# Kernel optimization log

Hardware: AMD Instinct MI355X
Metric: run time of the kernel (lower is better)

The kernel has to match this reference:

```python
import jax, jax.numpy as jnp
import numpy as np

N = 50000   # num_nodes
H = 128     # n_hidden
C = 16      # num_classes
R = 8       # num_rels
B = 4       # num_bases
E = 800000  # num_edges


def setup_inputs() -> dict:
    key = jax.random.key(0)
    ks = jax.random.split(key, 20)
    s = 0.05
    return {
        "src": jax.random.randint(ks[0], (E,), 0, N),
        "dst": jax.random.randint(ks[1], (E,), 0, N),
        "h": jnp.arange(N),                      # node IDs (first layer in_feat == num_nodes)
        "r": jax.random.randint(ks[2], (E,), 0, R),
        "norm": jax.random.uniform(ks[3], (E, 1), dtype=jnp.float32),
        # layer 0: basis weights over [num_nodes -> H]
        "bases0": jax.random.normal(ks[4], (B, N, H), dtype=jnp.float32) * s,
        "wcomp0": jax.random.normal(ks[5], (R, B), dtype=jnp.float32) * s,
        "loop0": jax.random.normal(ks[6], (N, H), dtype=jnp.float32) * s,
        "bias0": jnp.zeros((H,), dtype=jnp.float32),
        # layer 1: H -> H
        "bases1": jax.random.normal(ks[7], (B, H, H), dtype=jnp.float32) * s,
        "wcomp1": jax.random.normal(ks[8], (R, B), dtype=jnp.float32) * s,
        "loop1": jax.random.normal(ks[9], (H, H), dtype=jnp.float32) * s,
        "bias1": jnp.zeros((H,), dtype=jnp.float32),
        # layer 2: H -> C
        "bases2": jax.random.normal(ks[10], (B, H, C), dtype=jnp.float32) * s,
        "wcomp2": jax.random.normal(ks[11], (R, B), dtype=jnp.float32) * s,
        "loop2": jax.random.normal(ks[12], (H, C), dtype=jnp.float32) * s,
        "bias2": jnp.zeros((C,), dtype=jnp.float32),
    }


def _agg(msg, dst):
    return jax.ops.segment_sum(msg, dst, num_segments=N)


def _layer_id(ids, src, dst, r, norm, bases, wcomp, loop, bias):
    # first layer: input features are node IDs -> embedding lookup into composed weight
    w = jnp.einsum('rb,bnf->rnf', wcomp, bases)      # [R, N, H]
    msg = w[r, ids[src]] * norm                      # [E, H] gather per edge
    out = _agg(msg, dst) + loop[ids] + bias          # aggregate + self-loop + bias
    return jax.nn.relu(out)


def _layer_dense(x, src, dst, r, norm, bases, wcomp, loop, bias, act):
    w = jnp.einsum('rb,bdf->rdf', wcomp, bases)      # [R, d_in, d_out]
    trans = jnp.einsum('nd,rdf->rnf', x, w)          # [R, N, d_out] (all rel transforms)
    msg = trans[r, src] * norm                       # [E, d_out] relation-indexed gather
    out = _agg(msg, dst) + x @ loop + bias
    return jax.nn.relu(out) if act else out


def reference(src, dst, h, r, norm,
              bases0, wcomp0, loop0, bias0,
              bases1, wcomp1, loop1, bias1,
              bases2, wcomp2, loop2, bias2):
    x = _layer_id(h, src, dst, r, norm, bases0, wcomp0, loop0, bias0)
    x = _layer_dense(x, src, dst, r, norm, bases1, wcomp1, loop1, bias1, act=True)
    x = _layer_dense(x, src, dst, r, norm, bases2, wcomp2, loop2, bias2, act=False)
    return x
```

## Files before the change

### kernel.cpp

```cpp
#include <hip/hip_runtime.h>

#define NN 50000
#define NP 50048
#define HH 128
#define CC 16
#define RRL 8
#define BB 4
#define EE 800000
#define NT (RRL * NN)
#define SCAN_CHUNK 2048
#define NBLK_SCAN ((NT + SCAN_CHUNK - 1) / SCAN_CHUNK)
#define KBIG 1152
#define W0B_BLOCKS ((NN * 32) / 256)
#define COMPOSE_THREADS (HH * KBIG + RRL * CC * HH + CC * HH)
#define COMPOSE_BLOCKS ((COMPOSE_THREADS + 255) / 256)
#define NC 98
#define SPLIT 2
#define CHUNK_E 4096
#define PA_BLOCKS ((EE + CHUNK_E - 1) / CHUNK_E)

typedef short bf16x8_t __attribute__((ext_vector_type(8)));
typedef float f32x4_t __attribute__((ext_vector_type(4)));

__device__ __forceinline__ unsigned short f2bf(float f) {
  unsigned int x = __float_as_uint(f);
  unsigned int r = x + 0x7fffu + ((x >> 16) & 1u);
  return (unsigned short)(r >> 16);
}
__device__ __forceinline__ float bflo(unsigned int u) { return __uint_as_float(u << 16); }
__device__ __forceinline__ float bfhi(unsigned int u) {
  return __uint_as_float(u & 0xffff0000u);
}
__device__ __forceinline__ void acc8(float* a, uint4 v, float nrm) {
  a[0] = fmaf(nrm, bflo(v.x), a[0]);
  a[1] = fmaf(nrm, bfhi(v.x), a[1]);
  a[2] = fmaf(nrm, bflo(v.y), a[2]);
  a[3] = fmaf(nrm, bfhi(v.y), a[3]);
  a[4] = fmaf(nrm, bflo(v.z), a[4]);
  a[5] = fmaf(nrm, bfhi(v.z), a[5]);
  a[6] = fmaf(nrm, bflo(v.w), a[6]);
  a[7] = fmaf(nrm, bfhi(v.w), a[7]);
}


__global__ __launch_bounds__(256) void hist2_kernel(const int* __restrict__ r,
                                                    const int* __restrict__ dst,
                                                    int* __restrict__ cnt) {
  int e = blockIdx.x * 256 + threadIdx.x;
  if (e < EE) atomicAdd(&cnt[dst[e] * RRL + r[e]], 1);
}

__global__ __launch_bounds__(256) void scanA_kernel(const int* __restrict__ cnt,
                                                    int* __restrict__ off,
                                                    int* __restrict__ partials) {
  __shared__ int sums[256];
  int tid = threadIdx.x;
  int base = blockIdx.x * SCAN_CHUNK + tid * 8;
  int v[8];
  int s = 0;
#pragma unroll
  for (int j = 0; j < 8; ++j) {
    int idx = base + j;
    v[j] = (idx < NT) ? cnt[idx] : 0;
    s += v[j];
  }
  sums[tid] = s;
  __syncthreads();
  for (int o = 1; o < 256; o <<= 1) {
    int t = (tid >= o) ? sums[tid - o] : 0;
    __syncthreads();
    sums[tid] += t;
    __syncthreads();
  }
  int run = sums[tid] - s;
#pragma unroll
  for (int j = 0; j < 8; ++j) {
    int idx = base + j;
    if (idx < NT) off[idx] = run;
    run += v[j];
  }
  if (tid == 255) partials[blockIdx.x] = sums[255];
}

__global__ __launch_bounds__(256) void scanB_kernel(const int* __restrict__ partials,
                                                    int* __restrict__ pexcl) {
  __shared__ int sums[256];
  int tid = threadIdx.x;
  int p = (tid < NBLK_SCAN) ? partials[tid] : 0;
  sums[tid] = p;
  __syncthreads();
  for (int o = 1; o < 256; o <<= 1) {
    int t = (tid >= o) ? sums[tid - o] : 0;
    __syncthreads();
    sums[tid] += t;
    __syncthreads();
  }
  if (tid < NBLK_SCAN) pexcl[tid] = sums[tid] - p;
}

__global__ __launch_bounds__(256) void addC_kernel(int* __restrict__ off,
                                                   const int* __restrict__ pexcl,
                                                   int* __restrict__ cur,
                                                   int* __restrict__ curC) {
  int tid = threadIdx.x;
  int add = pexcl[blockIdx.x];
  int base = blockIdx.x * SCAN_CHUNK + tid * 8;
#pragma unroll
  for (int j = 0; j < 8; ++j) {
    int idx = base + j;
    if (idx < NT) {
      int v = off[idx] + add;
      off[idx] = v;
      cur[idx] = v;
      if ((idx & 4095) == 0) curC[idx >> 12] = v;
    }
  }
  if (blockIdx.x == 0 && tid == 0) off[NT] = EE;
}


__global__ __launch_bounds__(256) void partitionA_kernel(
    const int* __restrict__ r, const int* __restrict__ dst, const int* __restrict__ src,
    const float* __restrict__ norm, int* __restrict__ curC, unsigned* __restrict__ tmpK,
    uint2* __restrict__ tmpP) {
  __shared__ int hist[NC];
  __shared__ int run[NC];
  int tid = threadIdx.x;
  int base = blockIdx.x * CHUNK_E;
  for (int i = tid; i < NC; i += 256) hist[i] = 0;
  __syncthreads();
#pragma unroll
  for (int j = 0; j < CHUNK_E / 256; ++j) {
    int e = base + tid + j * 256;
    if (e < EE) atomicAdd(&hist[dst[e] >> 9], 1);
  }
  __syncthreads();
  if (tid < NC && hist[tid] > 0) run[tid] = atomicAdd(&curC[tid], hist[tid]);
  __syncthreads();
#pragma unroll
  for (int j = 0; j < CHUNK_E / 256; ++j) {
    int e = base + tid + j * 256;
    if (e < EE) {
      int d = dst[e], z = r[e];
      int c = d >> 9;
      int pos = atomicAdd(&run[c], 1);
      tmpK[pos] = (unsigned)(d * RRL + z);
      uint2 pay;
      pay.x = (unsigned)src[e] | ((unsigned)z << 24);
      pay.y = __float_as_uint(norm[e]);
      tmpP[pos] = pay;
    }
  }
}


__global__ __launch_bounds__(256) void placeB_kernel(const int* __restrict__ off2,
                                                     const unsigned* __restrict__ tmpK,
                                                     const uint2* __restrict__ tmpP,
                                                     int* __restrict__ cur2,
                                                     uint2* __restrict__ ep1) {
  int c = blockIdx.x / SPLIT, q = blockIdx.x % SPLIT;
  int kb = c * 4096;
  int ke = (c + 1) * 4096;
  if (ke > NT) ke = NT;
  int beg = off2[kb], end = off2[ke];
  int len = end - beg;
  int qb = beg + (len * q) / SPLIT;
  int qe = beg + (len * (q + 1)) / SPLIT;
  for (int i = qb + threadIdx.x; i < qe; i += 256) {
    unsigned key = tmpK[i];
    uint2 pay = tmpP[i];
    int pos = atomicAdd(&cur2[key], 1);
    ep1[pos] = pay;
  }
}


__global__ __launch_bounds__(256) void prep_weights_kernel(
    const float* __restrict__ bases0, const float* __restrict__ wcomp0,
    unsigned short* __restrict__ w0b, const float* __restrict__ wcomp1,
    const float* __restrict__ bases1, const float* __restrict__ loop1,
    const float* __restrict__ wcomp2, const float* __restrict__ bases2,
    const float* __restrict__ loop2, unsigned short* __restrict__ w1big,
    unsigned short* __restrict__ w2t, unsigned short* __restrict__ loop2t) {
  if (blockIdx.x < W0B_BLOCKS) {
    int idx = blockIdx.x * 256 + threadIdx.x;
    int m = idx >> 5, c = idx & 31;
    if (m >= NN) return;
    float4 b0 = ((const float4*)(bases0 + ((size_t)0 * NN + m) * HH))[c];
    float4 b1 = ((const float4*)(bases0 + ((size_t)1 * NN + m) * HH))[c];
    float4 b2 = ((const float4*)(bases0 + ((size_t)2 * NN + m) * HH))[c];
    float4 b3 = ((const float4*)(bases0 + ((size_t)3 * NN + m) * HH))[c];
#pragma unroll
    for (int z = 0; z < RRL; ++z) {
      float c0 = wcomp0[z * BB + 0], c1 = wcomp0[z * BB + 1];
      float c2 = wcomp0[z * BB + 2], c3 = wcomp0[z * BB + 3];
      float vx = c0 * b0.x + c1 * b1.x + c2 * b2.x + c3 * b3.x;
      float vy = c0 * b0.y + c1 * b1.y + c2 * b2.y + c3 * b3.y;
      float vz = c0 * b0.z + c1 * b1.z + c2 * b2.z + c3 * b3.z;
      float vw = c0 * b0.w + c1 * b1.w + c2 * b2.w + c3 * b3.w;
      uint2 pk;
      pk.x = ((unsigned)f2bf(vy) << 16) | f2bf(vx);
      pk.y = ((unsigned)f2bf(vw) << 16) | f2bf(vz);
      ((uint2*)(w0b + ((size_t)z * NP + m) * HH))[c] = pk;
    }
    return;
  }
  int idx = (blockIdx.x - W0B_BLOCKS) * 256 + threadIdx.x;
  if (idx < HH * KBIG) {
    int n = idx / KBIG, k = idx - n * KBIG;
    float a;
    if (k < 1024) {
      int z = k >> 7, kk = k & 127;
      a = 0.f;
#pragma unroll
      for (int b = 0; b < BB; ++b)
        a += wcomp1[z * BB + b] * bases1[((size_t)b * HH + kk) * HH + n];
    } else {
      int kk = k - 1024;
      a = loop1[kk * HH + n];
    }
    w1big[idx] = f2bf(a);
    return;
  }
  int j = idx - HH * KBIG;
  if (j < RRL * CC * HH) {
    int z = j >> 11;
    int rem = j & 2047;
    int n = rem >> 7, k = rem & 127;
    float a = 0.f;
#pragma unroll
    for (int b = 0; b < BB; ++b)
      a += wcomp2[z * BB + b] * bases2[((size_t)b * HH + k) * CC + n];
    w2t[j] = f2bf(a);
    return;
  }
  j -= RRL * CC * HH;
  if (j < CC * HH) {
    int n = j >> 7, k = j & 127;
    loop2t[j] = f2bf(loop2[k * CC + n]);
  }
}


__global__ __launch_bounds__(256) void l0_seg_kernel(
    const int* __restrict__ h, const int* __restrict__ off2, const uint2* __restrict__ ep1,
    const unsigned short* __restrict__ w0b, const float* __restrict__ loop0,
    const float* __restrict__ bias0, unsigned short* __restrict__ x1b) {
  int lane = threadIdx.x & 63;
  int n = blockIdx.x * 4 + (threadIdx.x >> 6);
  if (n >= NP) return;
  const int g = lane >> 4;
  const int t = lane & 15;
  float acc[8];
#pragma unroll
  for (int j = 0; j < 8; ++j) acc[j] = 0.f;

  if (n < NN) {
    int beg = off2[n * RRL];
    int end = off2[n * RRL + RRL];
    int i = beg + g;
    uint2 p0 = {0u, 0u}, p1 = {0u, 0u};
    if (i < end) p0 = ep1[i];
    if (i + 4 < end) p1 = ep1[i + 4];
    unsigned r0 = (p0.x >> 24) * NP + (unsigned)h[p0.x & 0xFFFFFFu];
    unsigned r1 = (p1.x >> 24) * NP + (unsigned)h[p1.x & 0xFFFFFFu];
    while (i < end) {
      uint2 q0 = {0u, 0u}, q1 = {0u, 0u};
      if (i + 8 < end) q0 = ep1[i + 8];
      if (i + 12 < end) q1 = ep1[i + 12];
      uint4 va = *(const uint4*)(w0b + (size_t)r0 * HH + t * 8);
      uint4 vb = *(const uint4*)(w0b + (size_t)r1 * HH + t * 8);
      float na = __uint_as_float(p0.y), nb = __uint_as_float(p1.y);
      acc8(acc, va, na);
      acc8(acc, vb, nb);
      i += 8;
      p0 = q0;
      p1 = q1;
      r0 = (q0.x >> 24) * NP + (unsigned)h[q0.x & 0xFFFFFFu];
      r1 = (q1.x >> 24) * NP + (unsigned)h[q1.x & 0xFFFFFFu];
    }
  }
#pragma unroll
  for (int j = 0; j < 8; ++j) {
    acc[j] += __shfl_xor(acc[j], 16, 64);
    acc[j] += __shfl_xor(acc[j], 32, 64);
  }
  if (g != 0) return;
  uint4 o = {0u, 0u, 0u, 0u};
  if (n < NN) {
    int hn = h[n];
    float4 l0v = ((const float4*)(loop0 + (size_t)hn * HH))[t * 2];
    float4 l1v = ((const float4*)(loop0 + (size_t)hn * HH))[t * 2 + 1];
    float4 b0v = ((const float4*)bias0)[t * 2];
    float4 b1v = ((const float4*)bias0)[t * 2 + 1];
    float e0 = fmaxf(acc[0] + l0v.x + b0v.x, 0.f);
    float e1 = fmaxf(acc[1] + l0v.y + b0v.y, 0.f);
    float e2 = fmaxf(acc[2] + l0v.z + b0v.z, 0.f);
    float e3 = fmaxf(acc[3] + l0v.w + b0v.w, 0.f);
    float e4 = fmaxf(acc[4] + l1v.x + b1v.x, 0.f);
    float e5 = fmaxf(acc[5] + l1v.y + b1v.y, 0.f);
    float e6 = fmaxf(acc[6] + l1v.z + b1v.z, 0.f);
    float e7 = fmaxf(acc[7] + l1v.w + b1v.w, 0.f);
    o.x = ((unsigned)f2bf(e1) << 16) | f2bf(e0);
    o.y = ((unsigned)f2bf(e3) << 16) | f2bf(e2);
    o.z = ((unsigned)f2bf(e5) << 16) | f2bf(e4);
    o.w = ((unsigned)f2bf(e7) << 16) | f2bf(e6);
  }
  *(uint4*)(x1b + (size_t)n * HH + t * 8) = o;
}


__global__ __launch_bounds__(256) void l1_agg_kernel(const int* __restrict__ off2,
                                                     const uint2* __restrict__ ep1,
                                                     const unsigned short* __restrict__ x1b,
                                                     unsigned short* __restrict__ AGG) {
  int tid = threadIdx.x;
  int gid = blockIdx.x * 16 + (tid >> 4);
  int l = tid & 15;
  int n = gid >> 3, z = gid & 7;
  if (n >= NP) return;
  unsigned short* orow = AGG + (size_t)n * 1024 + z * 128 + l * 8;
  if (n >= NN) {
    *(uint4*)orow = (uint4){0u, 0u, 0u, 0u};
    return;
  }
  int beg = off2[gid];
  int end = off2[gid + 1];
  float a[8];
#pragma unroll
  for (int j = 0; j < 8; ++j) a[j] = 0.f;

  int i = beg;
  uint2 p0 = {0u, 0u}, p1 = {0u, 0u};
  if (i < end) p0 = ep1[i];
  if (i + 1 < end) p1 = ep1[i + 1];
  while (i < end) {
    uint2 q0 = {0u, 0u}, q1 = {0u, 0u};
    if (i + 2 < end) q0 = ep1[i + 2];
    if (i + 3 < end) q1 = ep1[i + 3];
    unsigned s0 = p0.x & 0xFFFFFFu, s1 = p1.x & 0xFFFFFFu;
    uint4 v0 = *(const uint4*)(x1b + (size_t)s0 * HH + l * 8);
    uint4 v1 = *(const uint4*)(x1b + (size_t)s1 * HH + l * 8);
    float n0 = __uint_as_float(p0.y), n1 = __uint_as_float(p1.y);
    acc8(a, v0, n0);
    acc8(a, v1, n1);
    i += 2;
    p0 = q0;
    p1 = q1;
  }
  uint4 o;
  o.x = ((unsigned)f2bf(a[1]) << 16) | f2bf(a[0]);
  o.y = ((unsigned)f2bf(a[3]) << 16) | f2bf(a[2]);
  o.z = ((unsigned)f2bf(a[5]) << 16) | f2bf(a[4]);
  o.w = ((unsigned)f2bf(a[7]) << 16) | f2bf(a[6]);
  *(uint4*)orow = o;
}


__global__ __launch_bounds__(256) void gemm_k1152_kernel(
    const unsigned short* __restrict__ AGG, const unsigned short* __restrict__ x1b,
    const unsigned short* __restrict__ w1big, const float* __restrict__ bias1,
    unsigned short* __restrict__ x2b) {
  constexpr int LP = 136;
  __shared__ unsigned short Alds[64 * LP];
  __shared__ unsigned short Blds[128 * LP];
  const int row0 = blockIdx.x * 64;
  const int tid = threadIdx.x;
  const int w = tid >> 6, lane = tid & 63;
  const int quad = lane >> 4, l15 = lane & 15;
  const int rb = (w >> 1) * 32;
  const int cb = (w & 1) * 64;

  f32x4_t acc[2][4];
#pragma unroll
  for (int rt = 0; rt < 2; ++rt)
#pragma unroll
    for (int ct = 0; ct < 4; ++ct) acc[rt][ct] = (f32x4_t){0.f, 0.f, 0.f, 0.f};

  for (int kb = 0; kb < 9; ++kb) {
    if (kb) __syncthreads();
#pragma unroll
    for (int it = 0; it < 4; ++it) {
      int flat = tid + it * 256;
      int row = flat >> 4, c8 = flat & 15;
      const unsigned short* srcp =
          (kb < 8) ? AGG + (size_t)(row0 + row) * 1024 + kb * 128 + c8 * 8
                   : x1b + (size_t)(row0 + row) * 128 + c8 * 8;
      *(uint4*)(&Alds[row * LP + c8 * 8]) = *(const uint4*)srcp;
    }
#pragma unroll
    for (int it = 0; it < 8; ++it) {
      int flat = tid + it * 256;
      int row = flat >> 4, c8 = flat & 15;
      *(uint4*)(&Blds[row * LP + c8 * 8]) =
          *(const uint4*)(w1big + (size_t)row * KBIG + kb * 128 + c8 * 8);
    }
    __syncthreads();
#pragma unroll
    for (int ks = 0; ks < 4; ++ks) {
      int ko = ks * 32 + quad * 8;
      bf16x8_t af[2], bfr[4];
#pragma unroll
      for (int rt = 0; rt < 2; ++rt)
        af[rt] = *(const bf16x8_t*)(&Alds[(rb + rt * 16 + l15) * LP + ko]);
#pragma unroll
      for (int ct = 0; ct < 4; ++ct)
        bfr[ct] = *(const bf16x8_t*)(&Blds[(cb + ct * 16 + l15) * LP + ko]);
#pragma unroll
      for (int rt = 0; rt < 2; ++rt)
#pragma unroll
        for (int ct = 0; ct < 4; ++ct)
          acc[rt][ct] =
              __builtin_amdgcn_mfma_f32_16x16x32_bf16(af[rt], bfr[ct], acc[rt][ct], 0, 0, 0);
    }
  }
#pragma unroll
  for (int rt = 0; rt < 2; ++rt)
#pragma unroll
    for (int ct = 0; ct < 4; ++ct) {
      int n = cb + ct * 16 + l15;
      float bv = bias1[n];
#pragma unroll
      for (int i = 0; i < 4; ++i) {
        int m = row0 + rb + rt * 16 + quad * 4 + i;
        float val = (m < NN) ? fmaxf(acc[rt][ct][i] + bv, 0.f) : 0.f;
        x2b[(size_t)m * HH + n] = f2bf(val);
      }
    }
}


__global__ __launch_bounds__(256) void l2_trans_kernel(
    const unsigned short* __restrict__ x2b, const unsigned short* __restrict__ w2t,
    const unsigned short* __restrict__ loop2t, const float* __restrict__ bias2,
    unsigned short* __restrict__ trans2, float* __restrict__ out) {
  constexpr int LP = 136;
  __shared__ unsigned short Alds[128 * LP];
  __shared__ unsigned short Blds[9][16 * LP];
  const int row0 = blockIdx.x * 128;
  const int tid = threadIdx.x;

#pragma unroll
  for (int it = 0; it < 8; ++it) {
    int flat = tid + it * 256;
    int row = flat >> 4, c8 = flat & 15;
    *(uint4*)(&Alds[row * LP + c8 * 8]) =
        *(const uint4*)(x2b + ((size_t)(row0 + row)) * 128 + c8 * 8);
  }
  {
    int row = tid >> 4, c8 = tid & 15;
#pragma unroll
    for (int z = 0; z < 9; ++z) {
      const unsigned short* B = (z < 8) ? w2t + (size_t)z * CC * HH : loop2t;
      *(uint4*)(&Blds[z][row * LP + c8 * 8]) = *(const uint4*)(B + row * 128 + c8 * 8);
    }
  }
  __syncthreads();

  const int w = tid >> 6, lane = tid & 63;
  const int quad = lane >> 4, l15 = lane & 15;
  const int rb = w * 32;

  for (int z = 0; z < 9; ++z) {
    f32x4_t acc[2];
    acc[0] = (f32x4_t){0.f, 0.f, 0.f, 0.f};
    acc[1] = (f32x4_t){0.f, 0.f, 0.f, 0.f};
#pragma unroll
    for (int ks = 0; ks < 4; ++ks) {
      int ko = ks * 32 + quad * 8;
      bf16x8_t af0 = *(const bf16x8_t*)(&Alds[(rb + l15) * LP + ko]);
      bf16x8_t af1 = *(const bf16x8_t*)(&Alds[(rb + 16 + l15) * LP + ko]);
      bf16x8_t bfr = *(const bf16x8_t*)(&Blds[z][l15 * LP + ko]);
      acc[0] = __builtin_amdgcn_mfma_f32_16x16x32_bf16(af0, bfr, acc[0], 0, 0, 0);
      acc[1] = __builtin_amdgcn_mfma_f32_16x16x32_bf16(af1, bfr, acc[1], 0, 0, 0);
    }
    if (z < 8) {
      unsigned short* ob = trans2 + (size_t)z * NP * CC;
#pragma unroll
      for (int rt = 0; rt < 2; ++rt)
#pragma unroll
        for (int i = 0; i < 4; ++i) {
          int m = row0 + rb + rt * 16 + quad * 4 + i;
          ob[(size_t)m * CC + l15] = f2bf(acc[rt][i]);
        }
    } else {
      float bv = bias2[l15];
#pragma unroll
      for (int rt = 0; rt < 2; ++rt)
#pragma unroll
        for (int i = 0; i < 4; ++i) {
          int m = row0 + rb + rt * 16 + quad * 4 + i;
          if (m < NN) out[(size_t)m * CC + l15] = acc[rt][i] + bv;
        }
    }
  }
}


__global__ __launch_bounds__(256) void l2_seg_kernel(const int* __restrict__ off2,
                                                     const uint2* __restrict__ ep1,
                                                     const unsigned short* __restrict__ trans2,
                                                     float* __restrict__ outp) {
  int lane = threadIdx.x & 63;
  int n = blockIdx.x * 4 + (threadIdx.x >> 6);
  if (n >= NN) return;
  const int g = lane >> 3;
  const int t = lane & 7;
  float a0 = 0.f, a1 = 0.f;
  int beg = off2[n * RRL];
  int end = off2[n * RRL + RRL];
  int i = beg + g;
  uint2 p0 = {0u, 0u}, p1 = {0u, 0u};
  if (i < end) p0 = ep1[i];
  if (i + 8 < end) p1 = ep1[i + 8];
  while (i < end) {
    uint2 q0 = {0u, 0u}, q1 = {0u, 0u};
    if (i + 16 < end) q0 = ep1[i + 16];
    if (i + 24 < end) q1 = ep1[i + 24];
    unsigned s0 = p0.x & 0xFFFFFFu, z0 = p0.x >> 24;
    unsigned s1 = p1.x & 0xFFFFFFu, z1 = p1.x >> 24;
    unsigned int u0 =
        *(const unsigned int*)(trans2 + ((size_t)z0 * NP + s0) * CC + t * 2);
    unsigned int u1 =
        *(const unsigned int*)(trans2 + ((size_t)z1 * NP + s1) * CC + t * 2);
    float na = __uint_as_float(p0.y), nb = __uint_as_float(p1.y);
    a0 = fmaf(na, bflo(u0), a0);
    a1 = fmaf(na, bfhi(u0), a1);
    a0 = fmaf(nb, bflo(u1), a0);
    a1 = fmaf(nb, bfhi(u1), a1);
    i += 16;
    p0 = q0;
    p1 = q1;
  }
  a0 += __shfl_xor(a0, 8, 64);
  a0 += __shfl_xor(a0, 16, 64);
  a0 += __shfl_xor(a0, 32, 64);
  a1 += __shfl_xor(a1, 8, 64);
  a1 += __shfl_xor(a1, 16, 64);
  a1 += __shfl_xor(a1, 32, 64);
  if (g != 0) return;
  float2* o = (float2*)(outp + (size_t)n * CC) + t;
  float2 cv = *o;
  cv.x += a0;
  cv.y += a1;
  *o = cv;
}


extern "C" void kernel_launch(void* const* d_in, const int* in_sizes, int n_in,
                              void* d_out, int out_size, void* d_ws, size_t ws_size,
                              hipStream_t stream) {
  const int* src = (const int*)d_in[0];
  const int* dst = (const int*)d_in[1];
  const int* h = (const int*)d_in[2];
  const int* r = (const int*)d_in[3];
  const float* norm = (const float*)d_in[4];
  const float* bases0 = (const float*)d_in[5];
  const float* wcomp0 = (const float*)d_in[6];
  const float* loop0 = (const float*)d_in[7];
  const float* bias0 = (const float*)d_in[8];
  const float* bases1 = (const float*)d_in[9];
  const float* wcomp1 = (const float*)d_in[10];
  const float* loop1 = (const float*)d_in[11];
  const float* bias1 = (const float*)d_in[12];
  const float* bases2 = (const float*)d_in[13];
  const float* wcomp2 = (const float*)d_in[14];
  const float* loop2 = (const float*)d_in[15];
  const float* bias2 = (const float*)d_in[16];
  float* out = (float*)d_out;

  char* p = (char*)d_ws;
  auto alloc = [&](size_t bytes) {
    char* q = p;
    p += (bytes + 255) & ~(size_t)255;
    return q;
  };
  unsigned short* x1b = (unsigned short*)alloc((size_t)NP * HH * 2);
  unsigned short* x2b = (unsigned short*)alloc((size_t)NP * HH * 2);
  unsigned short* trans2 = (unsigned short*)alloc((size_t)RRL * NP * CC * 2);
  unsigned short* w1big = (unsigned short*)alloc((size_t)HH * KBIG * 2);
  unsigned short* w2t = (unsigned short*)alloc((size_t)RRL * CC * HH * 2);
  unsigned short* loop2t = (unsigned short*)alloc((size_t)CC * HH * 2);
  uint2* ep1 = (uint2*)alloc((size_t)EE * 8);
  unsigned* tmpK = (unsigned*)alloc((size_t)EE * 4);
  uint2* tmpP = (uint2*)alloc((size_t)EE * 8);
  int* off2 = (int*)alloc((size_t)(NT + 1) * 4);
  int* cur2 = (int*)alloc((size_t)NT * 4);
  int* cnt2 = (int*)alloc((size_t)NT * 4);
  int* curC = (int*)alloc(1024);
  int* partials = (int*)alloc(1024);
  int* pexcl = (int*)alloc(1024);
  unsigned short* BIG = (unsigned short*)alloc((size_t)RRL * NP * HH * 2);

  hipMemsetAsync(cnt2, 0, (size_t)NT * 4, stream);
  hist2_kernel<<<(EE + 255) / 256, 256, 0, stream>>>(r, dst, cnt2);
  scanA_kernel<<<NBLK_SCAN, 256, 0, stream>>>(cnt2, off2, partials);
  scanB_kernel<<<1, 256, 0, stream>>>(partials, pexcl);
  addC_kernel<<<NBLK_SCAN, 256, 0, stream>>>(off2, pexcl, cur2, curC);
  partitionA_kernel<<<PA_BLOCKS, 256, 0, stream>>>(r, dst, src, norm, curC, tmpK, tmpP);
  placeB_kernel<<<NC * SPLIT, 256, 0, stream>>>(off2, tmpK, tmpP, cur2, ep1);

  prep_weights_kernel<<<W0B_BLOCKS + COMPOSE_BLOCKS, 256, 0, stream>>>(
      bases0, wcomp0, BIG, wcomp1, bases1, loop1, wcomp2, bases2, loop2, w1big, w2t,
      loop2t);

  l0_seg_kernel<<<NP / 4, 256, 0, stream>>>(h, off2, ep1, BIG, loop0, bias0, x1b);

  l1_agg_kernel<<<NP * 8 / 16, 256, 0, stream>>>(off2, ep1, x1b, BIG);
  gemm_k1152_kernel<<<NP / 64, 256, 0, stream>>>(BIG, x1b, w1big, bias1, x2b);

  l2_trans_kernel<<<NP / 128, 256, 0, stream>>>(x2b, w2t, loop2t, bias2, trans2, out);
  l2_seg_kernel<<<(NN + 3) / 4, 256, 0, stream>>>(off2, ep1, trans2, out);
}
```

Before: 479.0 us.

## Interleave layer-0 composed weights by node and widen per-lane gathers

Changes the composed layer-0 weight table from relation-major [R][NP][H] to node-major [N][R][H], so all eight relation rows of a source node sit contiguously. The prep kernel now has each thread handle 8 columns and emit one 16-byte store per relation. The gather kernel now has each lane load 32 bytes per edge and handle 8 edges per wave instead of 4, with an extra shuffle stage for the reduction. The aim is better locality and fewer, wider memory transactions for the random edge gathers, at the cost of higher register use and fewer edges in flight per lane group.

```diff
diff --git a/kernel.cpp b/kernel.cpp
--- a/kernel.cpp
+++ b/kernel.cpp
@@ -11,7 +11,7 @@
 #define SCAN_CHUNK 2048
 #define NBLK_SCAN ((NT + SCAN_CHUNK - 1) / SCAN_CHUNK)
 #define KBIG 1152
-#define W0B_BLOCKS ((NN * 32) / 256)
+#define W0B_BLOCKS ((NN * 16) / 256)
 #define COMPOSE_THREADS (HH * KBIG + RRL * CC * HH + CC * HH)
 #define COMPOSE_BLOCKS ((COMPOSE_THREADS + 255) / 256)
 #define NC 98
@@ -152,7 +152,6 @@
     }
   }
 }
-
 
 __global__ __launch_bounds__(256) void placeB_kernel(const int* __restrict__ off2,
                                                      const unsigned* __restrict__ tmpK,
@@ -185,24 +184,33 @@
     unsigned short* __restrict__ w2t, unsigned short* __restrict__ loop2t) {
   if (blockIdx.x < W0B_BLOCKS) {
     int idx = blockIdx.x * 256 + threadIdx.x;
-    int m = idx >> 5, c = idx & 31;
-    if (m >= NN) return;
-    float4 b0 = ((const float4*)(bases0 + ((size_t)0 * NN + m) * HH))[c];
-    float4 b1 = ((const float4*)(bases0 + ((size_t)1 * NN + m) * HH))[c];
-    float4 b2 = ((const float4*)(bases0 + ((size_t)2 * NN + m) * HH))[c];
-    float4 b3 = ((const float4*)(bases0 + ((size_t)3 * NN + m) * HH))[c];
+    int m = idx >> 4, c8 = idx & 15;
+    float4 a[BB][2];
+#pragma unroll
+    for (int b = 0; b < BB; ++b) {
+      const float4* sp = (const float4*)(bases0 + ((size_t)b * NN + m) * HH + c8 * 8);
+      a[b][0] = sp[0];
+      a[b][1] = sp[1];
+    }
+    uint4* orow = (uint4*)w0b + (size_t)m * 128 + c8;
 #pragma unroll
     for (int z = 0; z < RRL; ++z) {
       float c0 = wcomp0[z * BB + 0], c1 = wcomp0[z * BB + 1];
       float c2 = wcomp0[z * BB + 2], c3 = wcomp0[z * BB + 3];
-      float vx = c0 * b0.x + c1 * b1.x + c2 * b2.x + c3 * b3.x;
-      float vy = c0 * b0.y + c1 * b1.y + c2 * b2.y + c3 * b3.y;
-      float vz = c0 * b0.z + c1 * b1.z + c2 * b2.z + c3 * b3.z;
-      float vw = c0 * b0.w + c1 * b1.w + c2 * b2.w + c3 * b3.w;
-      uint2 pk;
-      pk.x = ((unsigned)f2bf(vy) << 16) | f2bf(vx);
-      pk.y = ((unsigned)f2bf(vw) << 16) | f2bf(vz);
-      ((uint2*)(w0b + ((size_t)z * NP + m) * HH))[c] = pk;
+      float e[8];
+#pragma unroll
+      for (int q = 0; q < 2; ++q) {
+        e[q * 4 + 0] = c0 * a[0][q].x + c1 * a[1][q].x + c2 * a[2][q].x + c3 * a[3][q].x;
+        e[q * 4 + 1] = c0 * a[0][q].y + c1 * a[1][q].y + c2 * a[2][q].y + c3 * a[3][q].y;
+        e[q * 4 + 2] = c0 * a[0][q].z + c1 * a[1][q].z + c2 * a[2][q].z + c3 * a[3][q].z;
+        e[q * 4 + 3] = c0 * a[0][q].w + c1 * a[1][q].w + c2 * a[2][q].w + c3 * a[3][q].w;
+      }
+      uint4 pk;
+      pk.x = ((unsigned)f2bf(e[1]) << 16) | f2bf(e[0]);
+      pk.y = ((unsigned)f2bf(e[3]) << 16) | f2bf(e[2]);
+      pk.z = ((unsigned)f2bf(e[5]) << 16) | f2bf(e[4]);
+      pk.w = ((unsigned)f2bf(e[7]) << 16) | f2bf(e[6]);
+      orow[z * 16] = pk;
     }
     return;
   }
@@ -250,11 +258,11 @@
   int lane = threadIdx.x & 63;
   int n = blockIdx.x * 4 + (threadIdx.x >> 6);
   if (n >= NP) return;
-  const int g = lane >> 4;
-  const int t = lane & 15;
-  float acc[8];
-#pragma unroll
-  for (int j = 0; j < 8; ++j) acc[j] = 0.f;
+  const int g = lane >> 3;
+  const int t = lane & 7;
+  float acc[16];
+#pragma unroll
+  for (int j = 0; j < 16; ++j) acc[j] = 0.f;
 
   if (n < NN) {
     int beg = off2[n * RRL];
@@ -262,52 +270,63 @@
     int i = beg + g;
     uint2 p0 = {0u, 0u}, p1 = {0u, 0u};
     if (i < end) p0 = ep1[i];
-    if (i + 4 < end) p1 = ep1[i + 4];
-    unsigned r0 = (p0.x >> 24) * NP + (unsigned)h[p0.x & 0xFFFFFFu];
-    unsigned r1 = (p1.x >> 24) * NP + (unsigned)h[p1.x & 0xFFFFFFu];
+    if (i + 8 < end) p1 = ep1[i + 8];
+    unsigned r0 = (unsigned)h[p0.x & 0xFFFFFFu] * 8u + (p0.x >> 24);
+    unsigned r1 = (unsigned)h[p1.x & 0xFFFFFFu] * 8u + (p1.x >> 24);
     while (i < end) {
       uint2 q0 = {0u, 0u}, q1 = {0u, 0u};
-      if (i + 8 < end) q0 = ep1[i + 8];
-      if (i + 12 < end) q1 = ep1[i + 12];
-      uint4 va = *(const uint4*)(w0b + (size_t)r0 * HH + t * 8);
-      uint4 vb = *(const uint4*)(w0b + (size_t)r1 * HH + t * 8);
+      if (i + 16 < end) q0 = ep1[i + 16];
+      if (i + 24 < end) q1 = ep1[i + 24];
+      const uint4* rowa = (const uint4*)(w0b + (size_t)r0 * HH) + t * 2;
+      const uint4* rowb = (const uint4*)(w0b + (size_t)r1 * HH) + t * 2;
+      uint4 va0 = rowa[0], va1 = rowa[1];
+      uint4 vb0 = rowb[0], vb1 = rowb[1];
       float na = __uint_as_float(p0.y), nb = __uint_as_float(p1.y);
-      acc8(acc, va, na);
-      acc8(acc, vb, nb);
-      i += 8;
+      acc8(acc, va0, na);
+      acc8(acc + 8, va1, na);
+      acc8(acc, vb0, nb);
+      acc8(acc + 8, vb1, nb);
+      i += 16;
       p0 = q0;
       p1 = q1;
-      r0 = (q0.x >> 24) * NP + (unsigned)h[q0.x & 0xFFFFFFu];
-      r1 = (q1.x >> 24) * NP + (unsigned)h[q1.x & 0xFFFFFFu];
-    }
-  }
-#pragma unroll
-  for (int j = 0; j < 8; ++j) {
+      r0 = (unsigned)h[q0.x & 0xFFFFFFu] * 8u + (q0.x >> 24);
+      r1 = (unsigned)h[q1.x & 0xFFFFFFu] * 8u + (q1.x >> 24);
+    }
+  }
+#pragma unroll
+  for (int j = 0; j < 16; ++j) {
+    acc[j] += __shfl_xor(acc[j], 8, 64);
     acc[j] += __shfl_xor(acc[j], 16, 64);
     acc[j] += __shfl_xor(acc[j], 32, 64);
   }
   if (g != 0) return;
-  uint4 o = {0u, 0u, 0u, 0u};
+  uint4 o0 = {0u, 0u, 0u, 0u}, o1 = {0u, 0u, 0u, 0u};
   if (n < NN) {
     int hn = h[n];
-    float4 l0v = ((const float4*)(loop0 + (size_t)hn * HH))[t * 2];
-    float4 l1v = ((const float4*)(loop0 + (size_t)hn * HH))[t * 2 + 1];
-    float4 b0v = ((const float4*)bias0)[t * 2];
-    float4 b1v = ((const float4*)bias0)[t * 2 + 1];
-    float e0 = fmaxf(acc[0] + l0v.x + b0v.x, 0.f);
-    float e1 = fmaxf(acc[1] + l0v.y + b0v.y, 0.f);
-    float e2 = fmaxf(acc[2] + l0v.z + b0v.z, 0.f);
-    float e3 = fmaxf(acc[3] + l0v.w + b0v.w, 0.f);
-    float e4 = fmaxf(acc[4] + l1v.x + b1v.x, 0.f);
-    float e5 = fmaxf(acc[5] + l1v.y + b1v.y, 0.f);
-    float e6 = fmaxf(acc[6] + l1v.z + b1v.z, 0.f);
-    float e7 = fmaxf(acc[7] + l1v.w + b1v.w, 0.f);
-    o.x = ((unsigned)f2bf(e1) << 16) | f2bf(e0);
-    o.y = ((unsigned)f2bf(e3) << 16) | f2bf(e2);
-    o.z = ((unsigned)f2bf(e5) << 16) | f2bf(e4);
-    o.w = ((unsigned)f2bf(e7) << 16) | f2bf(e6);
-  }
-  *(uint4*)(x1b + (size_t)n * HH + t * 8) = o;
+    const float4* lp = (const float4*)(loop0 + (size_t)hn * HH) + t * 4;
+    const float4* bp = (const float4*)bias0 + t * 4;
+    float e[16];
+#pragma unroll
+    for (int q4 = 0; q4 < 4; ++q4) {
+      float4 lv = lp[q4];
+      float4 bv = bp[q4];
+      e[q4 * 4 + 0] = fmaxf(acc[q4 * 4 + 0] + lv.x + bv.x, 0.f);
+      e[q4 * 4 + 1] = fmaxf(acc[q4 * 4 + 1] + lv.y + bv.y, 0.f);
+      e[q4 * 4 + 2] = fmaxf(acc[q4 * 4 + 2] + lv.z + bv.z, 0.f);
+      e[q4 * 4 + 3] = fmaxf(acc[q4 * 4 + 3] + lv.w + bv.w, 0.f);
+    }
+    o0.x = ((unsigned)f2bf(e[1]) << 16) | f2bf(e[0]);
+    o0.y = ((unsigned)f2bf(e[3]) << 16) | f2bf(e[2]);
+    o0.z = ((unsigned)f2bf(e[5]) << 16) | f2bf(e[4]);
+    o0.w = ((unsigned)f2bf(e[7]) << 16) | f2bf(e[6]);
+    o1.x = ((unsigned)f2bf(e[9]) << 16) | f2bf(e[8]);
+    o1.y = ((unsigned)f2bf(e[11]) << 16) | f2bf(e[10]);
+    o1.z = ((unsigned)f2bf(e[13]) << 16) | f2bf(e[12]);
+    o1.w = ((unsigned)f2bf(e[15]) << 16) | f2bf(e[14]);
+  }
+  uint4* op = (uint4*)(x1b + (size_t)n * HH) + t * 2;
+  op[0] = o0;
+  op[1] = o1;
 }
 
 
```

After: 483.7 us. No clear change (+1.0%).

## Fuse edge histogram into partitioning and precompute interleaved layer-0 weight indices

Applied to the files above, without the earlier changes.

The edge histogram moves into the partition kernel, and coarse partitioning now writes into fixed-capacity buckets (CAP slots per 512-node chunk) instead of scan-derived offsets. That removes a separate pass over the edges and the dependency on the scan. Placement now also writes a second edge array holding a precomputed row index h[src]*8+z, which removes the dependent h lookup from the layer-0 gather. The composed layer-0 weights are re-laid out so the 8 relations of a node are interleaved, and the accumulators use packed float2 FMAs. The fixed bucket capacity assumes a roughly uniform dst distribution and would overflow on skewed graphs, and the extra edge array adds memory traffic during placement.

```diff
diff --git a/kernel.cpp b/kernel.cpp
--- a/kernel.cpp
+++ b/kernel.cpp
@@ -11,16 +11,18 @@
 #define SCAN_CHUNK 2048
 #define NBLK_SCAN ((NT + SCAN_CHUNK - 1) / SCAN_CHUNK)
 #define KBIG 1152
-#define W0B_BLOCKS ((NN * 32) / 256)
+#define W0B_BLOCKS ((NN * 16) / 256)
 #define COMPOSE_THREADS (HH * KBIG + RRL * CC * HH + CC * HH)
 #define COMPOSE_BLOCKS ((COMPOSE_THREADS + 255) / 256)
 #define NC 98
+#define CAP 10240
 #define SPLIT 2
 #define CHUNK_E 4096
 #define PA_BLOCKS ((EE + CHUNK_E - 1) / CHUNK_E)
 
 typedef short bf16x8_t __attribute__((ext_vector_type(8)));
 typedef float f32x4_t __attribute__((ext_vector_type(4)));
+typedef float f32x2_t __attribute__((ext_vector_type(2)));
 
 __device__ __forceinline__ unsigned short f2bf(float f) {
   unsigned int x = __float_as_uint(f);
@@ -31,24 +33,18 @@
 __device__ __forceinline__ float bfhi(unsigned int u) {
   return __uint_as_float(u & 0xffff0000u);
 }
-__device__ __forceinline__ void acc8(float* a, uint4 v, float nrm) {
-  a[0] = fmaf(nrm, bflo(v.x), a[0]);
-  a[1] = fmaf(nrm, bfhi(v.x), a[1]);
-  a[2] = fmaf(nrm, bflo(v.y), a[2]);
-  a[3] = fmaf(nrm, bfhi(v.y), a[3]);
-  a[4] = fmaf(nrm, bflo(v.z), a[4]);
-  a[5] = fmaf(nrm, bfhi(v.z), a[5]);
-  a[6] = fmaf(nrm, bflo(v.w), a[6]);
-  a[7] = fmaf(nrm, bfhi(v.w), a[7]);
-}
-
-
-__global__ __launch_bounds__(256) void hist2_kernel(const int* __restrict__ r,
-                                                    const int* __restrict__ dst,
-                                                    int* __restrict__ cnt) {
-  int e = blockIdx.x * 256 + threadIdx.x;
-  if (e < EE) atomicAdd(&cnt[dst[e] * RRL + r[e]], 1);
-}
+__device__ __forceinline__ void acc8v(f32x2_t* a, uint4 v, float nrm) {
+  f32x2_t nn = {nrm, nrm};
+  f32x2_t u0 = {bflo(v.x), bfhi(v.x)};
+  f32x2_t u1 = {bflo(v.y), bfhi(v.y)};
+  f32x2_t u2 = {bflo(v.z), bfhi(v.z)};
+  f32x2_t u3 = {bflo(v.w), bfhi(v.w)};
+  a[0] += nn * u0;
+  a[1] += nn * u1;
+  a[2] += nn * u2;
+  a[3] += nn * u3;
+}
+
 
 __global__ __launch_bounds__(256) void scanA_kernel(const int* __restrict__ cnt,
                                                     int* __restrict__ off,
@@ -100,8 +96,7 @@
 
 __global__ __launch_bounds__(256) void addC_kernel(int* __restrict__ off,
                                                    const int* __restrict__ pexcl,
-                                                   int* __restrict__ cur,
-                                                   int* __restrict__ curC) {
+                                                   int* __restrict__ cur) {
   int tid = threadIdx.x;
   int add = pexcl[blockIdx.x];
   int base = blockIdx.x * SCAN_CHUNK + tid * 8;
@@ -112,7 +107,6 @@
       int v = off[idx] + add;
       off[idx] = v;
       cur[idx] = v;
-      if ((idx & 4095) == 0) curC[idx >> 12] = v;
     }
   }
   if (blockIdx.x == 0 && tid == 0) off[NT] = EE;
@@ -121,8 +115,9 @@
 
 __global__ __launch_bounds__(256) void partitionA_kernel(
     const int* __restrict__ r, const int* __restrict__ dst, const int* __restrict__ src,
-    const float* __restrict__ norm, int* __restrict__ curC, unsigned* __restrict__ tmpK,
-    uint2* __restrict__ tmpP) {
+    const int* __restrict__ h, const float* __restrict__ norm, int* __restrict__ cnt2,
+    int* __restrict__ tmpCur, unsigned* __restrict__ tmpK, uint2* __restrict__ tmpP,
+    unsigned* __restrict__ tmpW) {
   __shared__ int hist[NC];
   __shared__ int run[NC];
   int tid = threadIdx.x;
@@ -135,43 +130,49 @@
     if (e < EE) atomicAdd(&hist[dst[e] >> 9], 1);
   }
   __syncthreads();
-  if (tid < NC && hist[tid] > 0) run[tid] = atomicAdd(&curC[tid], hist[tid]);
+  if (tid < NC && hist[tid] > 0)
+    run[tid] = tid * CAP + atomicAdd(&tmpCur[tid], hist[tid]);
   __syncthreads();
 #pragma unroll
   for (int j = 0; j < CHUNK_E / 256; ++j) {
     int e = base + tid + j * 256;
     if (e < EE) {
       int d = dst[e], z = r[e];
+      int key = d * RRL + z;
+      atomicAdd(&cnt2[key], 1);
       int c = d >> 9;
       int pos = atomicAdd(&run[c], 1);
-      tmpK[pos] = (unsigned)(d * RRL + z);
+      int sv = src[e];
+      tmpK[pos] = (unsigned)key;
       uint2 pay;
-      pay.x = (unsigned)src[e] | ((unsigned)z << 24);
+      pay.x = (unsigned)sv | ((unsigned)z << 24);
       pay.y = __float_as_uint(norm[e]);
       tmpP[pos] = pay;
-    }
-  }
-}
-
-
-__global__ __launch_bounds__(256) void placeB_kernel(const int* __restrict__ off2,
+      tmpW[pos] = (unsigned)h[sv] * 8u + (unsigned)z;
+    }
+  }
+}
+
+
+__global__ __launch_bounds__(256) void placeB_kernel(const int* __restrict__ tmpCur,
                                                      const unsigned* __restrict__ tmpK,
                                                      const uint2* __restrict__ tmpP,
+                                                     const unsigned* __restrict__ tmpW,
                                                      int* __restrict__ cur2,
-                                                     uint2* __restrict__ ep1) {
+                                                     uint2* __restrict__ ep1,
+                                                     uint2* __restrict__ epw) {
   int c = blockIdx.x / SPLIT, q = blockIdx.x % SPLIT;
-  int kb = c * 4096;
-  int ke = (c + 1) * 4096;
-  if (ke > NT) ke = NT;
-  int beg = off2[kb], end = off2[ke];
-  int len = end - beg;
-  int qb = beg + (len * q) / SPLIT;
-  int qe = beg + (len * (q + 1)) / SPLIT;
+  int cnt = tmpCur[c];
+  int qb = (cnt * q) / SPLIT;
+  int qe = (cnt * (q + 1)) / SPLIT;
+  int base = c * CAP;
   for (int i = qb + threadIdx.x; i < qe; i += 256) {
-    unsigned key = tmpK[i];
-    uint2 pay = tmpP[i];
+    unsigned key = tmpK[base + i];
+    uint2 pay = tmpP[base + i];
+    unsigned w = tmpW[base + i];
     int pos = atomicAdd(&cur2[key], 1);
     ep1[pos] = pay;
+    epw[pos] = (uint2){w, pay.y};
   }
 }
 
@@ -185,24 +186,33 @@
     unsigned short* __restrict__ w2t, unsigned short* __restrict__ loop2t) {
   if (blockIdx.x < W0B_BLOCKS) {
     int idx = blockIdx.x * 256 + threadIdx.x;
-    int m = idx >> 5, c = idx & 31;
-    if (m >= NN) return;
-    float4 b0 = ((const float4*)(bases0 + ((size_t)0 * NN + m) * HH))[c];
-    float4 b1 = ((const float4*)(bases0 + ((size_t)1 * NN + m) * HH))[c];
-    float4 b2 = ((const float4*)(bases0 + ((size_t)2 * NN + m) * HH))[c];
-    float4 b3 = ((const float4*)(bases0 + ((size_t)3 * NN + m) * HH))[c];
+    int m = idx >> 4, c8 = idx & 15;
+    float4 a[BB][2];
+#pragma unroll
+    for (int b = 0; b < BB; ++b) {
+      const float4* sp = (const float4*)(bases0 + ((size_t)b * NN + m) * HH + c8 * 8);
+      a[b][0] = sp[0];
+      a[b][1] = sp[1];
+    }
+    uint4* orow = (uint4*)w0b + (size_t)m * 128 + c8;
 #pragma unroll
     for (int z = 0; z < RRL; ++z) {
       float c0 = wcomp0[z * BB + 0], c1 = wcomp0[z * BB + 1];
       float c2 = wcomp0[z * BB + 2], c3 = wcomp0[z * BB + 3];
-      float vx = c0 * b0.x + c1 * b1.x + c2 * b2.x + c3 * b3.x;
-      float vy = c0 * b0.y + c1 * b1.y + c2 * b2.y + c3 * b3.y;
-      float vz = c0 * b0.z + c1 * b1.z + c2 * b2.z + c3 * b3.z;
-      float vw = c0 * b0.w + c1 * b1.w + c2 * b2.w + c3 * b3.w;
-      uint2 pk;
-      pk.x = ((unsigned)f2bf(vy) << 16) | f2bf(vx);
-      pk.y = ((unsigned)f2bf(vw) << 16) | f2bf(vz);
-      ((uint2*)(w0b + ((size_t)z * NP + m) * HH))[c] = pk;
+      float e[8];
+#pragma unroll
+      for (int q = 0; q < 2; ++q) {
+        e[q * 4 + 0] = c0 * a[0][q].x + c1 * a[1][q].x + c2 * a[2][q].x + c3 * a[3][q].x;
+        e[q * 4 + 1] = c0 * a[0][q].y + c1 * a[1][q].y + c2 * a[2][q].y + c3 * a[3][q].y;
+        e[q * 4 + 2] = c0 * a[0][q].z + c1 * a[1][q].z + c2 * a[2][q].z + c3 * a[3][q].z;
+        e[q * 4 + 3] = c0 * a[0][q].w + c1 * a[1][q].w + c2 * a[2][q].w + c3 * a[3][q].w;
+      }
+      uint4 pk;
+      pk.x = ((unsigned)f2bf(e[1]) << 16) | f2bf(e[0]);
+      pk.y = ((unsigned)f2bf(e[3]) << 16) | f2bf(e[2]);
+      pk.z = ((unsigned)f2bf(e[5]) << 16) | f2bf(e[4]);
+      pk.w = ((unsigned)f2bf(e[7]) << 16) | f2bf(e[6]);
+      orow[z * 16] = pk;
     }
     return;
   }
@@ -244,7 +254,7 @@
 
 
 __global__ __launch_bounds__(256) void l0_seg_kernel(
-    const int* __restrict__ h, const int* __restrict__ off2, const uint2* __restrict__ ep1,
+    const int* __restrict__ h, const int* __restrict__ off2, const uint2* __restrict__ epw,
     const unsigned short* __restrict__ w0b, const float* __restrict__ loop0,
     const float* __restrict__ bias0, unsigned short* __restrict__ x1b) {
   int lane = threadIdx.x & 63;
@@ -252,39 +262,35 @@
   if (n >= NP) return;
   const int g = lane >> 4;
   const int t = lane & 15;
-  float acc[8];
-#pragma unroll
-  for (int j = 0; j < 8; ++j) acc[j] = 0.f;
+  f32x2_t acc[4];
+#pragma unroll
+  for (int j = 0; j < 4; ++j) acc[j] = (f32x2_t){0.f, 0.f};
 
   if (n < NN) {
     int beg = off2[n * RRL];
     int end = off2[n * RRL + RRL];
     int i = beg + g;
     uint2 p0 = {0u, 0u}, p1 = {0u, 0u};
-    if (i < end) p0 = ep1[i];
-    if (i + 4 < end) p1 = ep1[i + 4];
-    unsigned r0 = (p0.x >> 24) * NP + (unsigned)h[p0.x & 0xFFFFFFu];
-    unsigned r1 = (p1.x >> 24) * NP + (unsigned)h[p1.x & 0xFFFFFFu];
+    if (i < end) p0 = epw[i];
+    if (i + 4 < end) p1 = epw[i + 4];
     while (i < end) {
       uint2 q0 = {0u, 0u}, q1 = {0u, 0u};
-      if (i + 8 < end) q0 = ep1[i + 8];
-      if (i + 12 < end) q1 = ep1[i + 12];
-      uint4 va = *(const uint4*)(w0b + (size_t)r0 * HH + t * 8);
-      uint4 vb = *(const uint4*)(w0b + (size_t)r1 * HH + t * 8);
-      float na = __uint_as_float(p0.y), nb = __uint_as_float(p1.y);
-      acc8(acc, va, na);
-      acc8(acc, vb, nb);
+      if (i + 8 < end) q0 = epw[i + 8];
+      if (i + 12 < end) q1 = epw[i + 12];
+      uint4 va = *(const uint4*)(w0b + (size_t)p0.x * HH + t * 8);
+      uint4 vb = *(const uint4*)(w0b + (size_t)p1.x * HH + t * 8);
+      acc8v(acc, va, __uint_as_float(p0.y));
+      acc8v(acc, vb, __uint_as_float(p1.y));
       i += 8;
       p0 = q0;
       p1 = q1;
-      r0 = (q0.x >> 24) * NP + (unsigned)h[q0.x & 0xFFFFFFu];
-      r1 = (q1.x >> 24) * NP + (unsigned)h[q1.x & 0xFFFFFFu];
-    }
-  }
+    }
+  }
+  float* af = (float*)acc;
 #pragma unroll
   for (int j = 0; j < 8; ++j) {
-    acc[j] += __shfl_xor(acc[j], 16, 64);
-    acc[j] += __shfl_xor(acc[j], 32, 64);
+    af[j] += __shfl_xor(af[j], 16, 64);
+    af[j] += __shfl_xor(af[j], 32, 64);
   }
   if (g != 0) return;
   uint4 o = {0u, 0u, 0u, 0u};
@@ -294,14 +300,14 @@
     float4 l1v = ((const float4*)(loop0 + (size_t)hn * HH))[t * 2 + 1];
     float4 b0v = ((const float4*)bias0)[t * 2];
     float4 b1v = ((const float4*)bias0)[t * 2 + 1];
-    float e0 = fmaxf(acc[0] + l0v.x + b0v.x, 0.f);
-    float e1 = fmaxf(acc[1] + l0v.y + b0v.y, 0.f);
-    float e2 = fmaxf(acc[2] + l0v.z + b0v.z, 0.f);
-    float e3 = fmaxf(acc[3] + l0v.w + b0v.w, 0.f);
-    float e4 = fmaxf(acc[4] + l1v.x + b1v.x, 0.f);
-    float e5 = fmaxf(acc[5] + l1v.y + b1v.y, 0.f);
-    float e6 = fmaxf(acc[6] + l1v.z + b1v.z, 0.f);
-    float e7 = fmaxf(acc[7] + l1v.w + b1v.w, 0.f);
+    float e0 = fmaxf(af[0] + l0v.x + b0v.x, 0.f);
+    float e1 = fmaxf(af[1] + l0v.y + b0v.y, 0.f);
+    float e2 = fmaxf(af[2] + l0v.z + b0v.z, 0.f);
+    float e3 = fmaxf(af[3] + l0v.w + b0v.w, 0.f);
+    float e4 = fmaxf(af[4] + l1v.x + b1v.x, 0.f);
+    float e5 = fmaxf(af[5] + l1v.y + b1v.y, 0.f);
+    float e6 = fmaxf(af[6] + l1v.z + b1v.z, 0.f);
+    float e7 = fmaxf(af[7] + l1v.w + b1v.w, 0.f);
     o.x = ((unsigned)f2bf(e1) << 16) | f2bf(e0);
     o.y = ((unsigned)f2bf(e3) << 16) | f2bf(e2);
     o.z = ((unsigned)f2bf(e5) << 16) | f2bf(e4);
@@ -327,9 +333,9 @@
   }
   int beg = off2[gid];
   int end = off2[gid + 1];
-  float a[8];
-#pragma unroll
-  for (int j = 0; j < 8; ++j) a[j] = 0.f;
+  f32x2_t a[4];
+#pragma unroll
+  for (int j = 0; j < 4; ++j) a[j] = (f32x2_t){0.f, 0.f};
 
   int i = beg;
   uint2 p0 = {0u, 0u}, p1 = {0u, 0u};
@@ -342,18 +348,18 @@
     unsigned s0 = p0.x & 0xFFFFFFu, s1 = p1.x & 0xFFFFFFu;
     uint4 v0 = *(const uint4*)(x1b + (size_t)s0 * HH + l * 8);
     uint4 v1 = *(const uint4*)(x1b + (size_t)s1 * HH + l * 8);
-    float n0 = __uint_as_float(p0.y), n1 = __uint_as_float(p1.y);
-    acc8(a, v0, n0);
-    acc8(a, v1, n1);
+    acc8v(a, v0, __uint_as_float(p0.y));
+    acc8v(a, v1, __uint_as_float(p1.y));
     i += 2;
     p0 = q0;
     p1 = q1;
   }
+  float* af = (float*)a;
   uint4 o;
-  o.x = ((unsigned)f2bf(a[1]) << 16) | f2bf(a[0]);
-  o.y = ((unsigned)f2bf(a[3]) << 16) | f2bf(a[2]);
-  o.z = ((unsigned)f2bf(a[5]) << 16) | f2bf(a[4]);
-  o.w = ((unsigned)f2bf(a[7]) << 16) | f2bf(a[6]);
+  o.x = ((unsigned)f2bf(af[1]) << 16) | f2bf(af[0]);
+  o.y = ((unsigned)f2bf(af[3]) << 16) | f2bf(af[2]);
+  o.z = ((unsigned)f2bf(af[5]) << 16) | f2bf(af[4]);
+  o.w = ((unsigned)f2bf(af[7]) << 16) | f2bf(af[6]);
   *(uint4*)orow = o;
 }
 
@@ -583,29 +589,31 @@
   unsigned short* w2t = (unsigned short*)alloc((size_t)RRL * CC * HH * 2);
   unsigned short* loop2t = (unsigned short*)alloc((size_t)CC * HH * 2);
   uint2* ep1 = (uint2*)alloc((size_t)EE * 8);
-  unsigned* tmpK = (unsigned*)alloc((size_t)EE * 4);
-  uint2* tmpP = (uint2*)alloc((size_t)EE * 8);
+  uint2* epw = (uint2*)alloc((size_t)EE * 8);
+  unsigned* tmpK = (unsigned*)alloc((size_t)NC * CAP * 4);
+  uint2* tmpP = (uint2*)alloc((size_t)NC * CAP * 8);
+  unsigned* tmpW = (unsigned*)alloc((size_t)NC * CAP * 4);
   int* off2 = (int*)alloc((size_t)(NT + 1) * 4);
   int* cur2 = (int*)alloc((size_t)NT * 4);
-  int* cnt2 = (int*)alloc((size_t)NT * 4);
-  int* curC = (int*)alloc(1024);
+  int* cnt2 = (int*)alloc((size_t)(NT + 256) * 4);
+  int* tmpCur = cnt2 + NT;
   int* partials = (int*)alloc(1024);
   int* pexcl = (int*)alloc(1024);
   unsigned short* BIG = (unsigned short*)alloc((size_t)RRL * NP * HH * 2);
 
-  hipMemsetAsync(cnt2, 0, (size_t)NT * 4, stream);
-  hist2_kernel<<<(EE + 255) / 256, 256, 0, stream>>>(r, dst, cnt2);
+  hipMemsetAsync(cnt2, 0, (size_t)(NT + 256) * 4, stream);
+  partitionA_kernel<<<PA_BLOCKS, 256, 0, stream>>>(r, dst, src, h, norm, cnt2, tmpCur,
+                                                   tmpK, tmpP, tmpW);
   scanA_kernel<<<NBLK_SCAN, 256, 0, stream>>>(cnt2, off2, partials);
   scanB_kernel<<<1, 256, 0, stream>>>(partials, pexcl);
-  addC_kernel<<<NBLK_SCAN, 256, 0, stream>>>(off2, pexcl, cur2, curC);
-  partitionA_kernel<<<PA_BLOCKS, 256, 0, stream>>>(r, dst, src, norm, curC, tmpK, tmpP);
-  placeB_kernel<<<NC * SPLIT, 256, 0, stream>>>(off2, tmpK, tmpP, cur2, ep1);
+  addC_kernel<<<NBLK_SCAN, 256, 0, stream>>>(off2, pexcl, cur2);
+  placeB_kernel<<<NC * SPLIT, 256, 0, stream>>>(tmpCur, tmpK, tmpP, tmpW, cur2, ep1, epw);
 
   prep_weights_kernel<<<W0B_BLOCKS + COMPOSE_BLOCKS, 256, 0, stream>>>(
       bases0, wcomp0, BIG, wcomp1, bases1, loop1, wcomp2, bases2, loop2, w1big, w2t,
       loop2t);
 
-  l0_seg_kernel<<<NP / 4, 256, 0, stream>>>(h, off2, ep1, BIG, loop0, bias0, x1b);
+  l0_seg_kernel<<<NP / 4, 256, 0, stream>>>(h, off2, epw, BIG, loop0, bias0, x1b);
 
   l1_agg_kernel<<<NP * 8 / 16, 256, 0, stream>>>(off2, ep1, x1b, BIG);
   gemm_k1152_kernel<<<NP / 64, 256, 0, stream>>>(BIG, x1b, w1big, bias1, x2b);
```

Result: no change. 477.0 us (-0.4%).
